# Optimization experiments

Hardware: AMD Instinct MI355X
Metric: run time of the kernel (lower is better)

Reference implementation:

```python
import jax, jax.numpy as jnp
import numpy as np

IN_F, OUT_F, K = 512, 512, 3
UP = 1
EPS = 1e-08
LR_MUL = 1.0
PAD = (K - 1) // 2
C_EQ = LR_MUL / np.sqrt(IN_F * K * K)  # EqualizedWeight scale


def setup_inputs() -> dict:
    key = jax.random.key(0)
    k1, k2, k3, k4 = jax.random.split(key, 4)
    b, h, w = 16, 64, 64
    x = jax.random.normal(k1, (b, IN_F, h, w), dtype=jnp.float32)
    s = jax.random.uniform(k2, (b, IN_F), dtype=jnp.float32)
    weight = jax.random.normal(k3, (OUT_F, IN_F, K, K), dtype=jnp.float32)
    bias = jax.random.normal(k4, (OUT_F,), dtype=jnp.float32)
    return {"x": x, "s": s, "weight": weight, "bias": bias}


def _conv_one(xi, wi):
    # xi: [c,h,w], wi: [out,in,k,k]
    out = jax.lax.conv_general_dilated(
        xi[None], wi,
        window_strides=(1, 1),
        padding=[(PAD, PAD), (PAD, PAD)],
        dimension_numbers=("NCHW", "OIHW", "NCHW"),
    )
    return out[0]


def reference(x, s, weight, bias):
    # modulate: [b,out,in,k,k]
    w = (weight * C_EQ)[None] * s[:, None, :, None, None]
    # demodulate
    sigma_inv = jax.lax.rsqrt(jnp.sum(w * w, axis=(2, 3, 4), keepdims=True) + EPS)
    w = w * sigma_inv
    # per-sample conv (equivalent to grouped conv with groups=b)
    out = jax.vmap(_conv_one)(x, w)  # [b,out,h,w]
    out = out + (bias * LR_MUL)[None, :, None, None]
    return out
```

## Files before the change

kernel.cpp:

```cpp
#include <hip/hip_runtime.h>
#include <cstdint>

typedef unsigned short u16;
typedef __bf16 bf16x8 __attribute__((ext_vector_type(8)));
typedef float f32x4 __attribute__((ext_vector_type(4)));

#define B_    16
#define CIN   512
#define COUT  512
#define HW_   64
#define PW    66
#define XH_ELEMS ((size_t)B_*PW*PW*CIN)
#define WA_ELEMS ((size_t)B_*16*9*COUT*32)

#define WAITV(N) asm volatile("s_waitcnt vmcnt(" #N ")" ::: "memory")

__device__ __forceinline__ u16 f2bf(float f) {
  union { float f; unsigned int u; } c; c.f = f;
  unsigned int u = c.u + 0x7fffu + ((c.u >> 16) & 1u);
  return (u16)(u >> 16);
}

__device__ __forceinline__ void async16(const void* g, void* l) {
  __builtin_amdgcn_global_load_lds(
      (__attribute__((address_space(1))) unsigned int*)(uintptr_t)g,
      (__attribute__((address_space(3))) unsigned int*)(uintptr_t)l,
      16, 0, 0);
}

__global__ __launch_bounds__(256) void zero_border(u16* __restrict__ xh) {
  int g = blockIdx.x * 256 + threadIdx.x;
  if (g >= B_ * 260 * 64) return;
  int c8 = g & 63;
  int t  = g >> 6;
  int b  = t / 260;
  int p  = t - b * 260;
  int rp, cp;
  if (p < 66)       { rp = 0;      cp = p; }
  else if (p < 132) { rp = 65;     cp = p - 66; }
  else {
    int q = p - 132;
    if (q < 64) { rp = q + 1;  cp = 0; }
    else        { rp = q - 63; cp = 65; }
  }
  u16* dst = xh + ((((size_t)b * PW + rp) * PW + cp) << 9) + (c8 << 3);
  *(uint4*)dst = make_uint4(0u, 0u, 0u, 0u);
}

__global__ __launch_bounds__(256) void transpose_x(const float* __restrict__ x,
                                                   u16* __restrict__ xh) {
  const int t   = threadIdx.x;
  const int c8  = t & 7;
  const int xq  = (t >> 3) & 15;
  const int y01 = t >> 7;
  const int i0  = blockIdx.x * 64;
  const int y   = blockIdx.y * 2 + y01;
  const int b   = blockIdx.z;

  float4 v[8];
#pragma unroll
  for (int k = 0; k < 8; ++k) {
    const int ci = i0 + c8 * 8 + k;
    v[k] = *(const float4*)(
        x + ((((size_t)b * CIN + ci) * HW_ + y) * HW_) + xq * 4);
  }
#pragma unroll
  for (int j = 0; j < 4; ++j) {
    const int xx = xq * 4 + j;
    u16 oc[8];
#pragma unroll
    for (int k = 0; k < 8; ++k) oc[k] = f2bf(v[k][j]);
    u16* dst = xh + ((((size_t)b * PW + (y + 1)) * PW + (xx + 1)) << 9)
                  + i0 + c8 * 8;
    *(uint4*)dst = *(uint4*)oc;
  }
}

__global__ __launch_bounds__(256) void sigma_kernel(const float* __restrict__ w,
                                                    const float* __restrict__ s,
                                                    float* __restrict__ sig) {
  __shared__ float row[CIN * 9];
  __shared__ float part[16][4];

  const int o   = blockIdx.x;
  const int tid = threadIdx.x;
  const int wv  = tid >> 6;
  const int lane = tid & 63;
  const float* wrow = w + (size_t)o * (CIN * 9);

#pragma unroll
  for (int it = 0; it < 5; ++it) {
    const int c = it * 256 + tid;
    if (c < 1152) *(float4*)&row[c * 4] = *(const float4*)(wrow + c * 4);
  }
  __syncthreads();

  float q0 = 0.f, q1 = 0.f;
#pragma unroll
  for (int tt = 0; tt < 9; ++tt) {
    const float a = row[(2 * tid) * 9 + tt];
    const float c = row[(2 * tid + 1) * 9 + tt];
    q0 += a * a; q1 += c * c;
  }

  const float C_EQ = 1.4731391e-2f;
#pragma unroll
  for (int b = 0; b < 16; ++b) {
    const float2 sv = *(const float2*)(s + (size_t)b * CIN + 2 * tid);
    float a = q0 * sv.x * sv.x + q1 * sv.y * sv.y;
#pragma unroll
    for (int off = 32; off > 0; off >>= 1) a += __shfl_xor(a, off, 64);
    if (lane == 0) part[b][wv] = a;
  }
  __syncthreads();
  if (tid < 16) {
    const float tot = part[tid][0] + part[tid][1] + part[tid][2] + part[tid][3];
    sig[(size_t)tid * COUT + o] = rsqrtf(tot * (C_EQ * C_EQ) + 1e-8f);
  }
}

__global__ __launch_bounds__(256) void scale_weights(const float* __restrict__ w,
                                                     const float* __restrict__ s,
                                                     const float* __restrict__ sig,
                                                     u16* __restrict__ wA) {
  __shared__ float wld[288][33];
  __shared__ float s2[32];
  __shared__ float si[32];

  const int tid = threadIdx.x;
  const int k   = blockIdx.x & 7;
  const int j   = blockIdx.x >> 3;
  const int oh  = (k << 1) | (j & 1);
  const int icc = (j >> 1) & 15;
  const int b   = j >> 5;
  const int o0  = oh << 5;

#pragma unroll
  for (int it = 0; it < 9; ++it) {
    const int c   = it * 256 + tid;
    const int ol  = c / 72;
    const int col = c - ol * 72;
    const float4 v = *(const float4*)(
        w + (size_t)(o0 + ol) * (CIN * 9) + icc * 288 + col * 4);
#pragma unroll
    for (int j2 = 0; j2 < 4; ++j2) wld[col * 4 + j2][ol] = v[j2];
  }
  if (tid < 32)      s2[tid] = 1.4731391e-2f * s[(size_t)b * CIN + icc * 32 + tid];
  else if (tid < 64) si[tid - 32] = sig[(size_t)b * COUT + o0 + (tid - 32)];
  __syncthreads();

  const int ol = tid >> 3;
  const int g4 = tid & 7;
  const float sg = si[ol];
  u16* base = wA + (size_t)b * (16 * 9 * COUT * 32);
#pragma unroll
  for (int tap = 0; tap < 9; ++tap) {
    u16 oc[4];
#pragma unroll
    for (int kk = 0; kk < 4; ++kk) {
      const int ich = g4 * 4 + kk;
      oc[kk] = f2bf(wld[ich * 9 + tap][ol] * s2[ich] * sg);
    }
    *(uint2*)(base + (((size_t)(icc * 9 + tap) * COUT) + o0 + ol) * 32 + g4 * 4)
        = *(uint2*)oc;
  }
}

#define AS_ELEMS (128 * 32)
#define BROWS    (6 * 66)
#define BS_ELEMS (BROWS * 32)

__device__ __forceinline__ void stage_A(const u16* __restrict__ wb,
                                        u16* dst, int phase, int o0, int tid) {
  const u16* asrc = wb + ((size_t)phase * COUT + o0) * 32;
#pragma unroll
  for (int t = 0; t < 2; ++t) {
    const int id   = t * 256 + tid;
    const int row  = id >> 2;
    const int slot = (id & 3) ^ (row & 3);
    async16(asrc + row * 32 + slot * 8, dst + id * 8);
  }
}

__device__ __forceinline__ void stage_B_slice(const u16* __restrict__ xb,
                                              u16* dst, int ic, int y0,
                                              int tid, int slice) {
  if (tid < 198) {
    const int id   = slice * 198 + tid;
    const int row  = id >> 2;
    const int slot = (id & 3) ^ (row & 3);
    async16(xb + ((size_t)y0 * PW + row) * CIN + ic * 32 + slot * 8,
            dst + id * 8);
  }
}

__global__ __launch_bounds__(256, 2) void modconv_mfma(const u16* __restrict__ xh,
                                                       const u16* __restrict__ wA,
                                                       const float* __restrict__ bias,
                                                       float* __restrict__ out) {
  __shared__ u16 As[3 * AS_ELEMS];
  __shared__ u16 Bs[2 * BS_ELEMS];

  const int tid  = threadIdx.x;
  const int lane = tid & 63;
  const int wv   = tid >> 6;
  const int l15  = lane & 15;
  const int q    = lane >> 4;
  const int sw15 = l15 & 3;

  const int lin     = blockIdx.x;
  const int logical = ((lin & 7) << 7) + (lin >> 3);
  const int yt = logical & 15;
  const int ot = (logical >> 4) & 3;
  const int b  = logical >> 6;
  const int y0 = yt << 2;
  const int o0 = ot << 7;

  const u16* xb = xh + (size_t)b * (PW * PW * CIN);
  const u16* wb = wA + (size_t)b * (16 * 9 * COUT * 32);

  f32x4 acc[8][4];
#pragma unroll
  for (int mi = 0; mi < 8; ++mi)
#pragma unroll
    for (int cg = 0; cg < 4; ++cg) acc[mi][cg] = (f32x4){0.f, 0.f, 0.f, 0.f};

#pragma unroll
  for (int sl = 0; sl < 8; ++sl) stage_B_slice(xb, Bs, 0, y0, tid, sl);
  stage_A(wb, As, 0, o0, tid);
  stage_A(wb, As + AS_ELEMS, 1, o0, tid);

  for (int ic = 0; ic < 15; ++ic) {
    const int bOff = (ic & 1) * BS_ELEMS;
    const int bNxt = BS_ELEMS - bOff;
#pragma unroll
    for (int tap = 0; tap < 9; ++tap) {
      if (tap == 0) { WAITV(2); } else { WAITV(3); }
      __builtin_amdgcn_s_barrier();
      __builtin_amdgcn_sched_barrier(0);

      const int ky = tap / 3, kx = tap % 3;
      const int aCur = (tap % 3) * AS_ELEMS;
      const int aDst = ((tap + 2) % 3) * AS_ELEMS;
      const int rbbase = (wv + ky) * 66 + kx;

      bf16x8 bfr[4];
#pragma unroll
      for (int cg = 0; cg < 4; ++cg) {
        const int rb = rbbase + cg * 16 + l15;
        bfr[cg] = *(const bf16x8*)
          &Bs[bOff + (rb << 5) + ((q ^ (rb & 3)) << 3)];
      }

      stage_A(wb, As + aDst, ic * 9 + tap + 2, o0, tid);
      if (tap < 8) stage_B_slice(xb, Bs + bNxt, ic + 1, y0, tid, tap);

      __builtin_amdgcn_s_setprio(1);
#pragma unroll
      for (int mi = 0; mi < 8; ++mi) {
        const int ra = (mi << 4) + l15;
        const bf16x8 af = *(const bf16x8*)
          &As[aCur + (ra << 5) + ((q ^ sw15) << 3)];
#pragma unroll
        for (int cg = 0; cg < 4; ++cg)
          acc[mi][cg] = __builtin_amdgcn_mfma_f32_16x16x32_bf16(
              af, bfr[cg], acc[mi][cg], 0, 0, 0);
      }
      __builtin_amdgcn_s_setprio(0);
    }
  }

  {
    const int bOff = BS_ELEMS;
#pragma unroll
    for (int tap = 0; tap < 9; ++tap) {
      if (tap < 8) { WAITV(2); } else { WAITV(0); }
      __builtin_amdgcn_s_barrier();
      __builtin_amdgcn_sched_barrier(0);

      const int ky = tap / 3, kx = tap % 3;
      const int aCur = (tap % 3) * AS_ELEMS;
      const int rbbase = (wv + ky) * 66 + kx;

      bf16x8 bfr[4];
#pragma unroll
      for (int cg = 0; cg < 4; ++cg) {
        const int rb = rbbase + cg * 16 + l15;
        bfr[cg] = *(const bf16x8*)
          &Bs[bOff + (rb << 5) + ((q ^ (rb & 3)) << 3)];
      }

      if (tap <= 6)
        stage_A(wb, As + ((tap + 2) % 3) * AS_ELEMS, 135 + tap + 2, o0, tid);

      __builtin_amdgcn_s_setprio(1);
#pragma unroll
      for (int mi = 0; mi < 8; ++mi) {
        const int ra = (mi << 4) + l15;
        const bf16x8 af = *(const bf16x8*)
          &As[aCur + (ra << 5) + ((q ^ sw15) << 3)];
#pragma unroll
        for (int cg = 0; cg < 4; ++cg)
          acc[mi][cg] = __builtin_amdgcn_mfma_f32_16x16x32_bf16(
              af, bfr[cg], acc[mi][cg], 0, 0, 0);
      }
      __builtin_amdgcn_s_setprio(0);
    }
  }

  const int y = y0 + wv;
#pragma unroll
  for (int mi = 0; mi < 8; ++mi) {
#pragma unroll
    for (int rg = 0; rg < 4; ++rg) {
      const int o = o0 + (mi << 4) + (q << 2) + rg;
      const float bv = bias[o];
      const size_t base = (((size_t)b * COUT + o) * HW_ + y) * HW_;
#pragma unroll
      for (int cg = 0; cg < 4; ++cg)
        out[base + (cg << 4) + l15] = acc[mi][cg][rg] + bv;
    }
  }
}

extern "C" void kernel_launch(void* const* d_in, const int* in_sizes, int n_in,
                              void* d_out, int out_size, void* d_ws, size_t ws_size,
                              hipStream_t stream) {
  const float* x    = (const float*)d_in[0];
  const float* s    = (const float*)d_in[1];
  const float* w    = (const float*)d_in[2];
  const float* bias = (const float*)d_in[3];
  float* out = (float*)d_out;

  u16* xh = (u16*)d_ws;
  u16* wA = xh + XH_ELEMS;
  float* sig = (float*)d_out;

  zero_border<<<(B_ * 260 * 64 + 255) / 256, 256, 0, stream>>>(xh);
  transpose_x<<<dim3(8, 32, 16), 256, 0, stream>>>(x, xh);
  sigma_kernel<<<512, 256, 0, stream>>>(w, s, sig);
  scale_weights<<<4096, 256, 0, stream>>>(w, s, sig, wA);
  modconv_mfma<<<1024, 256, 0, stream>>>(xh, wA, bias, out);
}
```

Measured before the change: 477.2 us.

## Move modulation into activations and demodulation into epilogue, share weights

The style scale s and the equalization constant are now folded into the bf16 activation transpose, and the demodulation factor sigma is applied per output channel in the GEMM epilogue. This lets a single bf16 weight layout be shared by all batch samples instead of building 16 per-sample scaled copies. The expected saving is the large scale_weights pass and the per-sample weight traffic, and the shared weights should hit more often in cache. Rounding changes because s is applied before bf16 conversion of x and sigma is applied after accumulation, and sig now lives in workspace rather than in the output buffer.

```diff
diff --git a/kernel.cpp b/kernel.cpp
--- a/kernel.cpp
+++ b/kernel.cpp
@@ -10,8 +10,8 @@
 #define COUT  512
 #define HW_   64
 #define PW    66
-#define XH_ELEMS ((size_t)B_*PW*PW*CIN)
-#define WA_ELEMS ((size_t)B_*16*9*COUT*32)
+#define XH_ELEMS  ((size_t)B_*PW*PW*CIN)
+#define WBF_ELEMS ((size_t)16*9*COUT*32)
 
 #define WAITV(N) asm volatile("s_waitcnt vmcnt(" #N ")" ::: "memory")
 
@@ -48,6 +48,7 @@
 }
 
 __global__ __launch_bounds__(256) void transpose_x(const float* __restrict__ x,
+                                                   const float* __restrict__ s,
                                                    u16* __restrict__ xh) {
   const int t   = threadIdx.x;
   const int c8  = t & 7;
@@ -57,6 +58,12 @@
   const int y   = blockIdx.y * 2 + y01;
   const int b   = blockIdx.z;
 
+  const float C_EQ = 1.4731391e-2f;
+  const float4 sA = *(const float4*)(s + (size_t)b * CIN + i0 + c8 * 8);
+  const float4 sB = *(const float4*)(s + (size_t)b * CIN + i0 + c8 * 8 + 4);
+  float cs[8] = {C_EQ * sA.x, C_EQ * sA.y, C_EQ * sA.z, C_EQ * sA.w,
+                 C_EQ * sB.x, C_EQ * sB.y, C_EQ * sB.z, C_EQ * sB.w};
+
   float4 v[8];
 #pragma unroll
   for (int k = 0; k < 8; ++k) {
@@ -69,7 +76,7 @@
     const int xx = xq * 4 + j;
     u16 oc[8];
 #pragma unroll
-    for (int k = 0; k < 8; ++k) oc[k] = f2bf(v[k][j]);
+    for (int k = 0; k < 8; ++k) oc[k] = f2bf(v[k][j] * cs[k]);
     u16* dst = xh + ((((size_t)b * PW + (y + 1)) * PW + (xx + 1)) << 9)
                   + i0 + c8 * 8;
     *(uint4*)dst = *(uint4*)oc;
@@ -119,20 +126,13 @@
   }
 }
 
-__global__ __launch_bounds__(256) void scale_weights(const float* __restrict__ w,
-                                                     const float* __restrict__ s,
-                                                     const float* __restrict__ sig,
-                                                     u16* __restrict__ wA) {
+__global__ __launch_bounds__(256) void wlayout(const float* __restrict__ w,
+                                               u16* __restrict__ wbf) {
   __shared__ float wld[288][33];
-  __shared__ float s2[32];
-  __shared__ float si[32];
 
   const int tid = threadIdx.x;
-  const int k   = blockIdx.x & 7;
-  const int j   = blockIdx.x >> 3;
-  const int oh  = (k << 1) | (j & 1);
-  const int icc = (j >> 1) & 15;
-  const int b   = j >> 5;
+  const int icc = blockIdx.x & 15;
+  const int oh  = blockIdx.x >> 4;
   const int o0  = oh << 5;
 
 #pragma unroll
@@ -145,23 +145,17 @@
 #pragma unroll
     for (int j2 = 0; j2 < 4; ++j2) wld[col * 4 + j2][ol] = v[j2];
   }
-  if (tid < 32)      s2[tid] = 1.4731391e-2f * s[(size_t)b * CIN + icc * 32 + tid];
-  else if (tid < 64) si[tid - 32] = sig[(size_t)b * COUT + o0 + (tid - 32)];
   __syncthreads();
 
   const int ol = tid >> 3;
   const int g4 = tid & 7;
-  const float sg = si[ol];
-  u16* base = wA + (size_t)b * (16 * 9 * COUT * 32);
 #pragma unroll
   for (int tap = 0; tap < 9; ++tap) {
     u16 oc[4];
 #pragma unroll
-    for (int kk = 0; kk < 4; ++kk) {
-      const int ich = g4 * 4 + kk;
-      oc[kk] = f2bf(wld[ich * 9 + tap][ol] * s2[ich] * sg);
-    }
-    *(uint2*)(base + (((size_t)(icc * 9 + tap) * COUT) + o0 + ol) * 32 + g4 * 4)
+    for (int kk = 0; kk < 4; ++kk)
+      oc[kk] = f2bf(wld[(g4 * 4 + kk) * 9 + tap][ol]);
+    *(uint2*)(wbf + (((size_t)(icc * 9 + tap) * COUT) + o0 + ol) * 32 + g4 * 4)
         = *(uint2*)oc;
   }
 }
@@ -195,7 +189,8 @@
 }
 
 __global__ __launch_bounds__(256, 2) void modconv_mfma(const u16* __restrict__ xh,
-                                                       const u16* __restrict__ wA,
+                                                       const u16* __restrict__ wbf,
+                                                       const float* __restrict__ sig,
                                                        const float* __restrict__ bias,
                                                        float* __restrict__ out) {
   __shared__ u16 As[3 * AS_ELEMS];
@@ -217,7 +212,7 @@
   const int o0 = ot << 7;
 
   const u16* xb = xh + (size_t)b * (PW * PW * CIN);
-  const u16* wb = wA + (size_t)b * (16 * 9 * COUT * 32);
+  const u16* wb = wbf;
 
   f32x4 acc[8][4];
 #pragma unroll
@@ -308,17 +303,19 @@
     }
   }
 
+  const float* sigrow = sig + (size_t)b * COUT;
   const int y = y0 + wv;
 #pragma unroll
   for (int mi = 0; mi < 8; ++mi) {
 #pragma unroll
     for (int rg = 0; rg < 4; ++rg) {
       const int o = o0 + (mi << 4) + (q << 2) + rg;
-      const float bv = bias[o];
+      const float sgv = sigrow[o];
+      const float bv  = bias[o];
       const size_t base = (((size_t)b * COUT + o) * HW_ + y) * HW_;
 #pragma unroll
       for (int cg = 0; cg < 4; ++cg)
-        out[base + (cg << 4) + l15] = acc[mi][cg][rg] + bv;
+        out[base + (cg << 4) + l15] = acc[mi][cg][rg] * sgv + bv;
     }
   }
 }
@@ -332,13 +329,13 @@
   const float* bias = (const float*)d_in[3];
   float* out = (float*)d_out;
 
-  u16* xh = (u16*)d_ws;
-  u16* wA = xh + XH_ELEMS;
-  float* sig = (float*)d_out;
+  u16* xh    = (u16*)d_ws;
+  u16* wbf   = xh + XH_ELEMS;
+  float* sig = (float*)(wbf + WBF_ELEMS);
 
   zero_border<<<(B_ * 260 * 64 + 255) / 256, 256, 0, stream>>>(xh);
-  transpose_x<<<dim3(8, 32, 16), 256, 0, stream>>>(x, xh);
+  transpose_x<<<dim3(8, 32, 16), 256, 0, stream>>>(x, s, xh);
   sigma_kernel<<<512, 256, 0, stream>>>(w, s, sig);
-  scale_weights<<<4096, 256, 0, stream>>>(w, s, sig, wA);
-  modconv_mfma<<<1024, 256, 0, stream>>>(xh, wA, bias, out);
-}
+  wlayout<<<256, 256, 0, stream>>>(w, wbf);
+  modconv_mfma<<<1024, 256, 0, stream>>>(xh, wbf, sig, bias, out);
+}
```

After: 458.8 us, median of 2. -3.9%, faster.
